# Kernel optimization log

Measured on AMD Instinct MI355X. Metric: run time of the kernel, lower is better.

Reference implementation:

```python
import jax, jax.numpy as jnp
import numpy as np

N = 50000
IN_CH = 8
HID = 64
OUT_CH = 2
H1 = 4  # heads in gat1
NEG_SLOPE = 0.2
EPS = 1e-16


def setup_inputs() -> dict:
    key = jax.random.key(0)
    ks = jax.random.split(key, 12)
    E = 800000
    x = jax.random.normal(ks[0], (N, IN_CH), dtype=jnp.float32)
    edge_index = jax.random.randint(ks[1], (2, E), 0, N, dtype=jnp.int64)
    # GATConv layer 1: in 8 -> 4 heads x 64, concat -> 256
    s1 = 1.0 / np.sqrt(IN_CH)
    W1 = jax.random.uniform(ks[2], (IN_CH, H1 * HID), jnp.float32, -s1, s1)
    a1_src = jax.random.uniform(ks[3], (H1, HID), jnp.float32, -0.1, 0.1)
    a1_dst = jax.random.uniform(ks[4], (H1, HID), jnp.float32, -0.1, 0.1)
    b1 = jnp.zeros((H1 * HID,), jnp.float32)
    # GATConv layer 2: in 256 -> 1 head x 64
    s2 = 1.0 / np.sqrt(H1 * HID)
    W2 = jax.random.uniform(ks[5], (H1 * HID, HID), jnp.float32, -s2, s2)
    a2_src = jax.random.uniform(ks[6], (1, HID), jnp.float32, -0.1, 0.1)
    a2_dst = jax.random.uniform(ks[7], (1, HID), jnp.float32, -0.1, 0.1)
    b2 = jnp.zeros((HID,), jnp.float32)
    # classifier 64 -> 2
    s3 = 1.0 / np.sqrt(HID)
    Wc = jax.random.uniform(ks[8], (HID, OUT_CH), jnp.float32, -s3, s3)
    bc = jnp.zeros((OUT_CH,), jnp.float32)
    return {
        "x": x, "edge_index": edge_index,
        "W1": W1, "a1_src": a1_src, "a1_dst": a1_dst, "b1": b1,
        "W2": W2, "a2_src": a2_src, "a2_dst": a2_dst, "b2": b2,
        "Wc": Wc, "bc": bc,
    }


def gat_conv(x, src, dst, W, a_src, a_dst, bias, heads, out_ch, concat):
    n = x.shape[0]
    h = (x @ W).reshape(n, heads, out_ch)  # [N,H,C]
    alpha_s = (h * a_src).sum(-1)  # [N,H]
    alpha_d = (h * a_dst).sum(-1)  # [N,H]
    e = alpha_s[src] + alpha_d[dst]  # [E,H]
    e = jnp.where(e > 0, e, NEG_SLOPE * e)  # leaky_relu
    # segment softmax over destination nodes
    m = jax.ops.segment_max(e, dst, num_segments=n)  # [N,H]
    ex = jnp.exp(e - m[dst])
    denom = jax.ops.segment_sum(ex, dst, num_segments=n)  # [N,H]
    alpha = ex / (denom[dst] + EPS)  # [E,H]
    msg = alpha[:, :, None] * h[src]  # [E,H,C]
    out = jax.ops.segment_sum(msg, dst, num_segments=n)  # [N,H,C]
    if concat:
        out = out.reshape(n, heads * out_ch)
    else:
        out = out.mean(axis=1)
    return out + bias


def reference(x, edge_index, W1, a1_src, a1_dst, b1, W2, a2_src, a2_dst, b2, Wc, bc):
    n = x.shape[0]
    loop = jnp.arange(n, dtype=edge_index.dtype)
    src = jnp.concatenate([edge_index[0], loop])
    dst = jnp.concatenate([edge_index[1], loop])
    # dropout p=0.3 is identity in eval mode
    h = gat_conv(x, src, dst, W1, a1_src, a1_dst, b1, H1, HID, concat=True)
    h = jax.nn.elu(h)
    h = gat_conv(h, src, dst, W2, a2_src, a2_dst, b2, 1, HID, concat=True)
    h = jax.nn.elu(h)
    return h @ Wc + bc
```

## Files before the change

kernel.cpp:

```cpp
#include <hip/hip_runtime.h>
#include <hip/hip_bf16.h>


typedef __attribute__((ext_vector_type(8))) short bf16x8;
typedef __attribute__((ext_vector_type(4))) float f32x4;

__device__ __forceinline__ float lrelu(float e) { return e > 0.f ? e : 0.2f * e; }
__device__ __forceinline__ float eluf(float v)  { return v > 0.f ? v : (__expf(v) - 1.f); }

__device__ __forceinline__ void split_bf16(float v, unsigned short& hi, unsigned short& lo) {
    __hip_bfloat16 h = __float2bfloat16(v);
    float hf = __bfloat162float(h);
    __hip_bfloat16 l = __float2bfloat16(v - hf);
    hi = *reinterpret_cast<unsigned short*>(&h);
    lo = *reinterpret_cast<unsigned short*>(&l);
}

__device__ __forceinline__ int detect_is64(const int* __restrict__ ei32, int* s_is64) {
    if (threadIdx.x < 64) {
        int w = ei32[2 * threadIdx.x + 1];
        unsigned long long b = __ballot(w != 0);
        if (threadIdx.x == 0) *s_is64 = (b == 0ull) ? 1 : 0;
    }
    __syncthreads();
    return *s_is64;
}

__global__ __launch_bounds__(256) void k1_alpha(
    const float* __restrict__ x, const float* __restrict__ W1,
    const float* __restrict__ a1s, const float* __restrict__ a1d,
    float* __restrict__ aS, float* __restrict__ aD, int* __restrict__ deg, int n) {
    __shared__ float sA1S[32], sA1D[32];
    int t = threadIdx.x;
    if (t < 64) {
        int k = (t & 31) >> 2, h = t & 3;
        const float* av = (t < 32) ? a1s : a1d;
        float ss = 0.f;
        for (int c = 0; c < 64; ++c)
            ss = fmaf(W1[k * 256 + h * 64 + c], av[h * 64 + c], ss);
        if (t < 32) sA1S[t] = ss; else sA1D[t - 32] = ss;
    }
    __syncthreads();
    int node = blockIdx.x * 256 + t;
    if (node >= n) return;
    deg[node] = 0;
    float4 xa = ((const float4*)x)[node * 2];
    float4 xb = ((const float4*)x)[node * 2 + 1];
    float xv[8] = {xa.x, xa.y, xa.z, xa.w, xb.x, xb.y, xb.z, xb.w};
    float s[4], d[4];
#pragma unroll
    for (int h = 0; h < 4; ++h) {
        float ss = 0.f, sd = 0.f;
#pragma unroll
        for (int k = 0; k < 8; ++k) {
            ss = fmaf(xv[k], sA1S[k * 4 + h], ss);
            sd = fmaf(xv[k], sA1D[k * 4 + h], sd);
        }
        s[h] = ss; d[h] = sd;
    }
    ((float4*)aS)[node] = make_float4(s[0], s[1], s[2], s[3]);
    ((float4*)aD)[node] = make_float4(d[0], d[1], d[2], d[3]);
}

__global__ __launch_bounds__(256) void kB_pack(
    const float* __restrict__ W2, uint4* __restrict__ Bpk) {
    int idx = blockIdx.x * 256 + threadIdx.x;
    int lane = idx & 63, rest = idx >> 6;
    int nt = rest & 3, ks = (rest >> 2) & 7, split = rest >> 5;
    unsigned short vals[8];
#pragma unroll
    for (int i = 0; i < 8; ++i) {
        int k = ks * 32 + (lane >> 4) * 8 + i;
        int col = nt * 16 + (lane & 15);
        unsigned short hi, lo;
        split_bf16(W2[k * 64 + col], hi, lo);
        vals[i] = split ? lo : hi;
    }
    uint4 w;
    w.x = (unsigned)vals[0] | ((unsigned)vals[1] << 16);
    w.y = (unsigned)vals[2] | ((unsigned)vals[3] << 16);
    w.z = (unsigned)vals[4] | ((unsigned)vals[5] << 16);
    w.w = (unsigned)vals[6] | ((unsigned)vals[7] << 16);
    Bpk[rest * 64 + lane] = w;
}

__global__ __launch_bounds__(256) void k2_count(
    const int* __restrict__ ei32, int E, int* __restrict__ deg) {
    __shared__ int sf;
    int is64 = detect_is64(ei32, &sf);
    int e = blockIdx.x * 256 + threadIdx.x;
    if (e < E) {
        int d = is64 ? ei32[(E + e) * 2] : ei32[E + e];
        atomicAdd(&deg[d], 1);
    }
}

__global__ __launch_bounds__(1024) void scan_block(
    const int* __restrict__ deg, int n, int* __restrict__ offs, int* __restrict__ bsum) {
    int t = threadIdx.x;
    int i = blockIdx.x * 1024 + t;
    int v = (i < n) ? deg[i] : 0;
    int lane = t & 63, w = t >> 6;
    int s = v;
#pragma unroll
    for (int off = 1; off < 64; off <<= 1) {
        int u = __shfl_up(s, off, 64);
        if (lane >= off) s += u;
    }
    __shared__ int wsums[16];
    if (lane == 63) wsums[w] = s;
    __syncthreads();
    if (t < 16) {
        int wv = wsums[t];
#pragma unroll
        for (int off = 1; off < 16; off <<= 1) {
            int u = __shfl_up(wv, off, 64);
            if (t >= off) wv += u;
        }
        wsums[t] = wv;
    }
    __syncthreads();
    int waveoff = (w == 0) ? 0 : wsums[w - 1];
    if (i < n) offs[i] = s + waveoff - v;
    if (t == 1023) bsum[blockIdx.x] = s + waveoff;
}

__global__ void scan_small(int* __restrict__ bsum, int nb) {
    int t = threadIdx.x;
    int v = (t < nb) ? bsum[t] : 0;
#pragma unroll
    for (int off = 1; off < 64; off <<= 1) {
        int u = __shfl_up(v, off, 64);
        if (t >= off) v += u;
    }
    if (t < nb) bsum[t] = v;
}

__global__ void scan_add(int* __restrict__ offs, const int* __restrict__ bsum,
                         int* __restrict__ cur, int n, int nb) {
    int i = blockIdx.x * blockDim.x + threadIdx.x;
    if (i < n) {
        int b = i >> 10;
        int val = offs[i] + (b ? bsum[b - 1] : 0);
        offs[i] = val;
        cur[i] = val;
    }
    if (i == 0) offs[n] = bsum[nb - 1];
}

__global__ __launch_bounds__(256) void k4_scatter(
    const int* __restrict__ ei32, int E, int* __restrict__ cur,
    int* __restrict__ ssrc) {
    __shared__ int sf;
    int is64 = detect_is64(ei32, &sf);
    int e = blockIdx.x * 256 + threadIdx.x;
    if (e < E) {
        int d = is64 ? ei32[(E + e) * 2] : ei32[E + e];
        int s = is64 ? ei32[e * 2] : ei32[e];
        int p = atomicAdd(&cur[d], 1);
        ssrc[p] = s;
    }
}

__global__ __launch_bounds__(256) void k5_agg1(
    const float* __restrict__ x, const float* __restrict__ aS,
    const float* __restrict__ aD, const int* __restrict__ offs,
    const int* __restrict__ ssrc, const float* __restrict__ W1,
    const float* __restrict__ b1, unsigned short* __restrict__ hhi,
    unsigned short* __restrict__ hlo, int n) {
    int node = blockIdx.x * 4 + (threadIdx.x >> 6);
    if (node >= n) return;
    int lane = threadIdx.x & 63;
    int h = lane & 3, eslot = lane >> 2;
    int s0 = offs[node], s1 = offs[node + 1];
    float ad = aD[node * 4 + h];
    float denom = 0.f;
    float vec[8] = {0.f, 0.f, 0.f, 0.f, 0.f, 0.f, 0.f, 0.f};
    const float4* xv = (const float4*)x;
    for (int e = s0 + eslot; e < s1; e += 16) {
        int s = ssrc[e];
        float ex = __expf(lrelu(aS[s * 4 + h] + ad));
        denom += ex;
        float4 xa = xv[s * 2];
        float4 xb = xv[s * 2 + 1];
        vec[0] = fmaf(ex, xa.x, vec[0]); vec[1] = fmaf(ex, xa.y, vec[1]);
        vec[2] = fmaf(ex, xa.z, vec[2]); vec[3] = fmaf(ex, xa.w, vec[3]);
        vec[4] = fmaf(ex, xb.x, vec[4]); vec[5] = fmaf(ex, xb.y, vec[5]);
        vec[6] = fmaf(ex, xb.z, vec[6]); vec[7] = fmaf(ex, xb.w, vec[7]);
    }
#pragma unroll
    for (int off = 4; off < 64; off <<= 1) {
        denom += __shfl_xor(denom, off, 64);
#pragma unroll
        for (int k = 0; k < 8; ++k) vec[k] += __shfl_xor(vec[k], off, 64);
    }
    float exs = __expf(lrelu(aS[node * 4 + h] + ad));
    denom += exs;
    float4 xa = xv[node * 2];
    float4 xb = xv[node * 2 + 1];
    vec[0] = fmaf(exs, xa.x, vec[0]); vec[1] = fmaf(exs, xa.y, vec[1]);
    vec[2] = fmaf(exs, xa.z, vec[2]); vec[3] = fmaf(exs, xa.w, vec[3]);
    vec[4] = fmaf(exs, xb.x, vec[4]); vec[5] = fmaf(exs, xb.y, vec[5]);
    vec[6] = fmaf(exs, xb.z, vec[6]); vec[7] = fmaf(exs, xb.w, vec[7]);
    float vhk[4][8], invd[4];
#pragma unroll
    for (int hh = 0; hh < 4; ++hh) {
        invd[hh] = 1.f / (__shfl(denom, hh, 64) + 1e-16f);
#pragma unroll
        for (int k = 0; k < 8; ++k) vhk[hh][k] = __shfl(vec[k], hh, 64);
    }
#pragma unroll
    for (int hh = 0; hh < 4; ++hh) {
        int j = hh * 64 + lane;
        float dot = 0.f;
#pragma unroll
        for (int k = 0; k < 8; ++k) dot = fmaf(vhk[hh][k], W1[k * 256 + j], dot);
        float o = eluf(fmaf(dot, invd[hh], b1[j]));
        unsigned short hi, lo;
        split_bf16(o, hi, lo);
        hhi[(size_t)node * 256 + j] = hi;
        hlo[(size_t)node * 256 + j] = lo;
    }
}

__global__ __launch_bounds__(256) void k6_mfma(
    const unsigned short* __restrict__ hhi, const unsigned short* __restrict__ hlo,
    const uint4* __restrict__ Bpk, const float* __restrict__ a2s,
    const float* __restrict__ a2d, float* __restrict__ h2,
    float* __restrict__ A2S, float* __restrict__ A2D, int n) {
    int lane = threadIdx.x & 63;
    int row0 = blockIdx.x * 64 + (threadIdx.x >> 6) * 16;
    int r = row0 + (lane & 15);
    if (r >= n) r = n - 1;
    f32x4 acc[4];
#pragma unroll
    for (int nt = 0; nt < 4; ++nt) acc[nt] = {0.f, 0.f, 0.f, 0.f};
#pragma unroll
    for (int ks = 0; ks < 8; ++ks) {
        int koff = ks * 32 + (lane >> 4) * 8;
        bf16x8 ahi = *(const bf16x8*)(hhi + (size_t)r * 256 + koff);
        bf16x8 alo = *(const bf16x8*)(hlo + (size_t)r * 256 + koff);
#pragma unroll
        for (int nt = 0; nt < 4; ++nt) {
            uint4 bh = Bpk[(ks * 4 + nt) * 64 + lane];
            uint4 bl = Bpk[((8 + ks) * 4 + nt) * 64 + lane];
            bf16x8 bhi = *(bf16x8*)&bh;
            bf16x8 blo = *(bf16x8*)&bl;
            acc[nt] = __builtin_amdgcn_mfma_f32_16x16x32_bf16(ahi, bhi, acc[nt], 0, 0, 0);
            acc[nt] = __builtin_amdgcn_mfma_f32_16x16x32_bf16(ahi, blo, acc[nt], 0, 0, 0);
            acc[nt] = __builtin_amdgcn_mfma_f32_16x16x32_bf16(alo, bhi, acc[nt], 0, 0, 0);
        }
    }
#pragma unroll
    for (int nt = 0; nt < 4; ++nt) {
#pragma unroll
        for (int reg = 0; reg < 4; ++reg) {
            int row = row0 + (lane >> 4) * 4 + reg;
            if (row < n) h2[(size_t)row * 64 + nt * 16 + (lane & 15)] = acc[nt][reg];
        }
    }
    float a2sv[4], a2dv[4];
#pragma unroll
    for (int nt = 0; nt < 4; ++nt) {
        a2sv[nt] = a2s[nt * 16 + (lane & 15)];
        a2dv[nt] = a2d[nt * 16 + (lane & 15)];
    }
#pragma unroll
    for (int reg = 0; reg < 4; ++reg) {
        float ps = 0.f, pd = 0.f;
#pragma unroll
        for (int nt = 0; nt < 4; ++nt) {
            ps = fmaf(acc[nt][reg], a2sv[nt], ps);
            pd = fmaf(acc[nt][reg], a2dv[nt], pd);
        }
#pragma unroll
        for (int off = 1; off < 16; off <<= 1) {
            ps += __shfl_xor(ps, off, 64);
            pd += __shfl_xor(pd, off, 64);
        }
        int row = row0 + (lane >> 4) * 4 + reg;
        if ((lane & 15) == 0 && row < n) { A2S[row] = ps; A2D[row] = pd; }
    }
}

__global__ __launch_bounds__(256) void k7_agg2(
    const float* __restrict__ h2, const float* __restrict__ A2S,
    const float* __restrict__ A2D, const int* __restrict__ offs,
    const int* __restrict__ ssrc, const float* __restrict__ b2,
    const float* __restrict__ Wc, const float* __restrict__ bc,
    float* __restrict__ out, int n) {
    int node = blockIdx.x * 4 + (threadIdx.x >> 6);
    if (node >= n) return;
    int c = threadIdx.x & 63;
    int s0 = offs[node], s1 = offs[node + 1];
    float ad = A2D[node];
    int g = c >> 4, q = c & 15;
    const float4* h2v = (const float4*)h2;
    float denom = 0.f;
    float4 acc = make_float4(0.f, 0.f, 0.f, 0.f);
    for (int e = s0 + g; e < s1; e += 4) {
        int s = ssrc[e];
        float4 hv = h2v[(size_t)s * 16 + q];
        float ex = __expf(lrelu(A2S[s] + ad));
        denom += ex;
        acc.x = fmaf(ex, hv.x, acc.x); acc.y = fmaf(ex, hv.y, acc.y);
        acc.z = fmaf(ex, hv.z, acc.z); acc.w = fmaf(ex, hv.w, acc.w);
    }
#pragma unroll
    for (int off = 16; off <= 32; off <<= 1) {
        denom += __shfl_xor(denom, off, 64);
        acc.x += __shfl_xor(acc.x, off, 64);
        acc.y += __shfl_xor(acc.y, off, 64);
        acc.z += __shfl_xor(acc.z, off, 64);
        acc.w += __shfl_xor(acc.w, off, 64);
    }
    float exs = __expf(lrelu(A2S[node] + ad));
    denom += exs;
    float4 hS = h2v[(size_t)node * 16 + q];
    acc.x = fmaf(exs, hS.x, acc.x); acc.y = fmaf(exs, hS.y, acc.y);
    acc.z = fmaf(exs, hS.z, acc.z); acc.w = fmaf(exs, hS.w, acc.w);
    float inv = 1.f / (denom + 1e-16f);
    float4 bv = ((const float4*)b2)[q];
    float o0 = eluf(fmaf(acc.x, inv, bv.x));
    float o1 = eluf(fmaf(acc.y, inv, bv.y));
    float o2 = eluf(fmaf(acc.z, inv, bv.z));
    float o3 = eluf(fmaf(acc.w, inv, bv.w));
    int ch = q * 4;
    float p0 = o0 * Wc[ch * 2 + 0] + o1 * Wc[ch * 2 + 2] + o2 * Wc[ch * 2 + 4] + o3 * Wc[ch * 2 + 6];
    float p1 = o0 * Wc[ch * 2 + 1] + o1 * Wc[ch * 2 + 3] + o2 * Wc[ch * 2 + 5] + o3 * Wc[ch * 2 + 7];
#pragma unroll
    for (int off = 8; off > 0; off >>= 1) {
        p0 += __shfl_xor(p0, off, 64);
        p1 += __shfl_xor(p1, off, 64);
    }
    if (c == 0) {
        out[(size_t)node * 2 + 0] = p0 + bc[0];
        out[(size_t)node * 2 + 1] = p1 + bc[1];
    }
}

extern "C" void kernel_launch(void* const* d_in, const int* in_sizes, int n_in,
                              void* d_out, int out_size, void* d_ws, size_t ws_size,
                              hipStream_t stream) {
    const float* x   = (const float*)d_in[0];
    const int*   ei  = (const int*)d_in[1];
    const float* W1  = (const float*)d_in[2];
    const float* a1s = (const float*)d_in[3];
    const float* a1d = (const float*)d_in[4];
    const float* b1  = (const float*)d_in[5];
    const float* W2  = (const float*)d_in[6];
    const float* a2s = (const float*)d_in[7];
    const float* a2d = (const float*)d_in[8];
    const float* b2  = (const float*)d_in[9];
    const float* Wc  = (const float*)d_in[10];
    const float* bc  = (const float*)d_in[11];
    float* out = (float*)d_out;
    (void)n_in; (void)out_size; (void)ws_size;

    int n = in_sizes[0] / 8;
    int E = in_sizes[1] / 2;

    char* ws = (char*)d_ws;
    size_t o = 0;
    auto carve = [&](size_t bytes) -> char* {
        char* p = ws + o;
        o = (o + bytes + 255) & ~(size_t)255;
        return p;
    };
    unsigned short* hhi = (unsigned short*)carve((size_t)n * 256 * 2);
    unsigned short* hlo = (unsigned short*)carve((size_t)n * 256 * 2);
    float* h2   = (float*)carve((size_t)n * 64 * 4);
    float* aS   = (float*)carve((size_t)n * 4 * 4);
    float* aD   = (float*)carve((size_t)n * 4 * 4);
    int*   deg  = (int*)carve((size_t)n * 4);
    int*   offs = (int*)carve((size_t)(n + 1) * 4);
    int*   cur  = (int*)carve((size_t)n * 4);
    int*   ssrc = (int*)carve((size_t)E * 4);
    int*   bsum = (int*)carve(64 * 4);
    uint4* Bpk  = (uint4*)carve(4096 * 16);
    float* A2S  = (float*)carve((size_t)n * 4);
    float* A2D  = (float*)carve((size_t)n * 4);

    k1_alpha<<<(n + 255) / 256, 256, 0, stream>>>(x, W1, a1s, a1d, aS, aD, deg, n);
    kB_pack<<<16, 256, 0, stream>>>(W2, Bpk);
    k2_count<<<(E + 255) / 256, 256, 0, stream>>>(ei, E, deg);
    int nb = (n + 1023) / 1024;
    scan_block<<<nb, 1024, 0, stream>>>(deg, n, offs, bsum);
    scan_small<<<1, 64, 0, stream>>>(bsum, nb);
    scan_add<<<(n + 255) / 256, 256, 0, stream>>>(offs, bsum, cur, n, nb);
    k4_scatter<<<(E + 255) / 256, 256, 0, stream>>>(ei, E, cur, ssrc);
    k5_agg1<<<(n + 3) / 4, 256, 0, stream>>>(x, aS, aD, offs, ssrc, W1, b1, hhi, hlo, n);
    k6_mfma<<<(n + 63) / 64, 256, 0, stream>>>(hhi, hlo, Bpk, a2s, a2d, h2, A2S, A2D, n);
    k7_agg2<<<(n + 3) / 4, 256, 0, stream>>>(h2, A2S, A2D, offs, ssrc, b2, Wc, bc, out, n);
}
```

Measured before the change: 275.7 us.

## Compact edge indices and range-partition count/scatter atomics by destination

Adds a compaction kernel that converts the int64 edge list into separate int32 dst/src arrays. The count and scatter kernels are relaunched with 8x as many blocks, each handling only destinations in one of 8 node ranges. This is meant to localise the atomic traffic on deg/cur to a smaller slice of memory per block so it stays cache-resident. In exchange every edge is read 8 times, and there is an extra kernel plus workspace.

```diff
diff --git a/kernel.cpp b/kernel.cpp
--- a/kernel.cpp
+++ b/kernel.cpp
@@ -84,14 +84,43 @@
     Bpk[rest * 64 + lane] = w;
 }
 
-__global__ __launch_bounds__(256) void k2_count(
-    const int* __restrict__ ei32, int E, int* __restrict__ deg) {
+__global__ __launch_bounds__(256) void kc_compact(
+    const int* __restrict__ ei32, int E, int* __restrict__ sdst,
+    int* __restrict__ ssrc0) {
     __shared__ int sf;
     int is64 = detect_is64(ei32, &sf);
-    int e = blockIdx.x * 256 + threadIdx.x;
-    if (e < E) {
-        int d = is64 ? ei32[(E + e) * 2] : ei32[E + e];
-        atomicAdd(&deg[d], 1);
+    int base = blockIdx.x * 2048 + threadIdx.x;
+#pragma unroll
+    for (int j = 0; j < 8; ++j) {
+        int e = base + j * 256;
+        if (e < E) {
+            if (is64) {
+                sdst[e] = ei32[(size_t)(E + e) * 2];
+                ssrc0[e] = ei32[(size_t)e * 2];
+            } else {
+                sdst[e] = ei32[E + e];
+                ssrc0[e] = ei32[e];
+            }
+        }
+    }
+}
+
+__device__ __forceinline__ int range_of(int d, int rpb) {
+    return (d >= rpb) + (d >= 2 * rpb) + (d >= 3 * rpb) + (d >= 4 * rpb)
+         + (d >= 5 * rpb) + (d >= 6 * rpb) + (d >= 7 * rpb);
+}
+
+__global__ __launch_bounds__(256) void k2r_count(
+    const int* __restrict__ sdst, int E, int rpb, int* __restrict__ deg) {
+    int rr = blockIdx.x & 7;
+    int base = (blockIdx.x >> 3) * 2048 + threadIdx.x;
+#pragma unroll
+    for (int j = 0; j < 8; ++j) {
+        int e = base + j * 256;
+        if (e < E) {
+            int d = sdst[e];
+            if (range_of(d, rpb) == rr) atomicAdd(&deg[d], 1);
+        }
     }
 }
 
@@ -148,17 +177,21 @@
     if (i == 0) offs[n] = bsum[nb - 1];
 }
 
-__global__ __launch_bounds__(256) void k4_scatter(
-    const int* __restrict__ ei32, int E, int* __restrict__ cur,
-    int* __restrict__ ssrc) {
-    __shared__ int sf;
-    int is64 = detect_is64(ei32, &sf);
-    int e = blockIdx.x * 256 + threadIdx.x;
-    if (e < E) {
-        int d = is64 ? ei32[(E + e) * 2] : ei32[E + e];
-        int s = is64 ? ei32[e * 2] : ei32[e];
-        int p = atomicAdd(&cur[d], 1);
-        ssrc[p] = s;
+__global__ __launch_bounds__(256) void k4r_scatter(
+    const int* __restrict__ sdst, const int* __restrict__ ssrc0, int E,
+    int rpb, int* __restrict__ cur, int* __restrict__ ssrc) {
+    int rr = blockIdx.x & 7;
+    int base = (blockIdx.x >> 3) * 2048 + threadIdx.x;
+#pragma unroll
+    for (int j = 0; j < 8; ++j) {
+        int e = base + j * 256;
+        if (e < E) {
+            int d = sdst[e];
+            if (range_of(d, rpb) == rr) {
+                int p = atomicAdd(&cur[d], 1);
+                ssrc[p] = ssrc0[e];
+            }
+        }
     }
 }
 
@@ -359,6 +392,7 @@
 
     int n = in_sizes[0] / 8;
     int E = in_sizes[1] / 2;
+    int rpb = (n + 7) / 8;
 
     char* ws = (char*)d_ws;
     size_t o = 0;
@@ -376,19 +410,23 @@
     int*   offs = (int*)carve((size_t)(n + 1) * 4);
     int*   cur  = (int*)carve((size_t)n * 4);
     int*   ssrc = (int*)carve((size_t)E * 4);
+    int*   sdst = (int*)carve((size_t)E * 4);
+    int*   ssrc0= (int*)carve((size_t)E * 4);
     int*   bsum = (int*)carve(64 * 4);
     uint4* Bpk  = (uint4*)carve(4096 * 16);
     float* A2S  = (float*)carve((size_t)n * 4);
     float* A2D  = (float*)carve((size_t)n * 4);
 
+    int nchunk = (E + 2047) / 2048;
     k1_alpha<<<(n + 255) / 256, 256, 0, stream>>>(x, W1, a1s, a1d, aS, aD, deg, n);
     kB_pack<<<16, 256, 0, stream>>>(W2, Bpk);
-    k2_count<<<(E + 255) / 256, 256, 0, stream>>>(ei, E, deg);
+    kc_compact<<<nchunk, 256, 0, stream>>>(ei, E, sdst, ssrc0);
+    k2r_count<<<nchunk * 8, 256, 0, stream>>>(sdst, E, rpb, deg);
     int nb = (n + 1023) / 1024;
     scan_block<<<nb, 1024, 0, stream>>>(deg, n, offs, bsum);
     scan_small<<<1, 64, 0, stream>>>(bsum, nb);
     scan_add<<<(n + 255) / 256, 256, 0, stream>>>(offs, bsum, cur, n, nb);
-    k4_scatter<<<(E + 255) / 256, 256, 0, stream>>>(ei, E, cur, ssrc);
+    k4r_scatter<<<nchunk * 8, 256, 0, stream>>>(sdst, ssrc0, E, rpb, cur, ssrc);
     k5_agg1<<<(n + 3) / 4, 256, 0, stream>>>(x, aS, aD, offs, ssrc, W1, b1, hhi, hlo, n);
     k6_mfma<<<(n + 63) / 64, 256, 0, stream>>>(hhi, hlo, Bpk, a2s, a2d, h2, A2S, A2D, n);
     k7_agg2<<<(n + 3) / 4, 256, 0, stream>>>(h2, A2S, A2D, offs, ssrc, b2, Wc, bc, out, n);
```

New measurement: 273.0 us. About the same (-1.0%).
